# Performance work log

Measured on AMD Instinct MI355X. Metric: run time of the kernel, lower is better.

Reference implementation:

```python
import jax, jax.numpy as jnp
import numpy as np

S, B, CLS = 14, 2, 20
L_COORD, L_NOOBJ = 5.0, 0.5
BATCH = 8192
C = 5 * B + CLS  # 30


def setup_inputs() -> dict:
    key = jax.random.key(0)
    k1, k2, k3 = jax.random.split(key, 3)
    pred = jax.random.normal(k1, (BATCH, S, S, C), dtype=jnp.float32)
    target = jax.random.uniform(k2, (BATCH, S, S, C), dtype=jnp.float32)
    # replicate the conf bit into both box slots (channels 4 and 9)
    obj = (jax.random.uniform(k3, (BATCH, S, S)) > 0.9).astype(jnp.float32)
    target = target.at[..., 4].set(obj)
    target = target.at[..., 9].set(obj)
    return {"pred": pred, "target": target}


def _decode(box5):
    # box5: [..., 5] = (cx, cy, sqrt_w, sqrt_h, conf) -> corners [..., 4]
    x, y, sw, sh = box5[..., 0], box5[..., 1], box5[..., 2], box5[..., 3]
    hw = 0.5 * sw * sw
    hh = 0.5 * sh * sh
    return jnp.stack([x - hw, y - hh, x + hw, y + hh], axis=-1)


def _iou(b1, b2):
    # elementwise IoU over matching rows, like compute_iou with N==M paired rows
    lt = jnp.maximum(b1[..., :2], b2[..., :2])
    rb = jnp.minimum(b1[..., 2:], b2[..., 2:])
    wh = jnp.maximum(rb - lt, 0.0)
    inter = wh[..., 0] * wh[..., 1]
    a1 = (b1[..., 2] - b1[..., 0]) * (b1[..., 3] - b1[..., 1])
    a2 = (b2[..., 2] - b2[..., 0]) * (b2[..., 3] - b2[..., 1])
    denom = a1 + a2 - inter
    safe = jnp.where(denom > 0, denom, 1.0)
    return jnp.where(denom > 0, inter / safe, 0.0)


def reference(pred, target):
    batch = pred.shape[0]
    p = pred.reshape(-1, C)    # [N, 30], N = batch*S*S
    t = target.reshape(-1, C)
    objf = (t[:, 4] > 0).astype(p.dtype)   # [N]
    noobjf = 1.0 - objf

    p_boxes = p[:, :5 * B].reshape(-1, B, 5)   # [N, B, 5]
    t_boxes = t[:, :5 * B].reshape(-1, B, 5)

    iou = _iou(_decode(t_boxes), _decode(p_boxes))   # [N, B]
    max_iou = jnp.max(iou, axis=1)                   # [N]
    max_idx = jnp.argmax(iou, axis=1)                # [N]
    sel = jax.nn.one_hot(max_idx, B, dtype=p.dtype)  # [N, B] response mask
    p_sel = jnp.einsum('nb,nbk->nk', sel, p_boxes)   # [N, 5] responsible pred box
    t_sel = jnp.einsum('nb,nbk->nk', sel, t_boxes)

    # localization: xy + sqrt-wh MSE on responsible box, obj cells only
    local = jnp.sum(objf[:, None] * (p_sel[:, :4] - t_sel[:, :4]) ** 2)
    # classification MSE, obj cells only
    cls_loss = jnp.sum(objf[:, None] * (p[:, 5 * B:] - t[:, 5 * B:]) ** 2)
    # containment: pred conf of responsible box vs (detached) max IoU
    miou_sg = jax.lax.stop_gradient(max_iou)
    contain = jnp.sum(objf * (p_sel[:, 4] - miou_sg) ** 2)
    # no-object: conf of all B boxes in empty cells
    noobj = jnp.sum(noobjf[:, None] * (p_boxes[:, :, 4] - t_boxes[:, :, 4]) ** 2)
    # iou loss: detached max IoU vs target conf of responsible box
    iou_loss = jnp.sum(objf * (miou_sg - t_sel[:, 4]) ** 2)

    loss_all = (L_COORD * local + cls_loss + contain
                + L_NOOBJ * noobj + iou_loss) / batch
    return loss_all
```

## Files before the change

kernel.cpp:

```cpp
#include <hip/hip_runtime.h>

#define SS 14
#define NBOX 2
#define NCLS 20
#define CCH 30

__global__ __launch_bounds__(256) void yolov1_loss_kernel(
    const float* __restrict__ pred, const float* __restrict__ target,
    float* __restrict__ out, int ncells, float inv_batch)
{
    float acc = 0.0f;
    int tid = blockIdx.x * blockDim.x + threadIdx.x;
    int stride = gridDim.x * blockDim.x;

    for (int cell = tid; cell < ncells; cell += stride) {
        const float2* pp = reinterpret_cast<const float2*>(pred + (size_t)cell * CCH);
        const float2* tp = reinterpret_cast<const float2*>(target + (size_t)cell * CCH);
        float p[CCH], t[CCH];
#pragma unroll
        for (int k = 0; k < CCH / 2; ++k) {
            float2 a = pp[k]; p[2 * k] = a.x; p[2 * k + 1] = a.y;
            float2 b = tp[k]; t[2 * k] = b.x; t[2 * k + 1] = b.y;
        }

        float iou0 = 0.f, iou1 = 0.f;
        float loc0 = 0.f, loc1 = 0.f;
#pragma unroll
        for (int b = 0; b < NBOX; ++b) {
            const int o = 5 * b;
            float thw = 0.5f * t[o + 2] * t[o + 2];
            float thh = 0.5f * t[o + 3] * t[o + 3];
            float phw = 0.5f * p[o + 2] * p[o + 2];
            float phh = 0.5f * p[o + 3] * p[o + 3];
            float t0x = t[o + 0] - thw, t0y = t[o + 1] - thh;
            float t1x = t[o + 0] + thw, t1y = t[o + 1] + thh;
            float p0x = p[o + 0] - phw, p0y = p[o + 1] - phh;
            float p1x = p[o + 0] + phw, p1y = p[o + 1] + phh;

            float ltx = fmaxf(t0x, p0x), lty = fmaxf(t0y, p0y);
            float rbx = fminf(t1x, p1x), rby = fminf(t1y, p1y);
            float w = fmaxf(rbx - ltx, 0.0f);
            float h = fmaxf(rby - lty, 0.0f);
            float inter = w * h;
            float a1 = (t1x - t0x) * (t1y - t0y);
            float a2 = (p1x - p0x) * (p1y - p0y);
            float denom = a1 + a2 - inter;
            float iou_b = (denom > 0.0f) ? (inter / denom) : 0.0f;

            float l = 0.0f;
#pragma unroll
            for (int k = 0; k < 4; ++k) {
                float d = p[o + k] - t[o + k];
                l += d * d;
            }
            if (b == 0) { iou0 = iou_b; loc0 = l; }
            else        { iou1 = iou_b; loc1 = l; }
        }

        int sel1 = (iou1 > iou0);
        float max_iou = fmaxf(iou0, iou1);
        float loc   = sel1 ? loc1   : loc0;
        float pconf = sel1 ? p[9]   : p[4];
        float tconf = sel1 ? t[9]   : t[4];

        float cls = 0.0f;
#pragma unroll
        for (int k = 5 * NBOX; k < CCH; ++k) {
            float d = p[k] - t[k];
            cls += d * d;
        }

        float dcon = pconf - max_iou;
        float d4 = p[4] - t[4];
        float d9 = p[9] - t[9];
        float noobj = d4 * d4 + d9 * d9;
        float diou = max_iou - tconf;

        float objf = (t[4] > 0.0f) ? 1.0f : 0.0f;
        acc += objf * (5.0f * loc + cls + dcon * dcon + diou * diou)
             + (1.0f - objf) * 0.5f * noobj;
    }

#pragma unroll
    for (int off = 32; off > 0; off >>= 1)
        acc += __shfl_down(acc, off, 64);

    __shared__ float wsum[4];
    int lane = threadIdx.x & 63;
    int wid = threadIdx.x >> 6;
    if (lane == 0) wsum[wid] = acc;
    __syncthreads();
    if (threadIdx.x == 0) {
        float s = wsum[0] + wsum[1] + wsum[2] + wsum[3];
        atomicAdd(out, s * inv_batch);
    }
}

extern "C" void kernel_launch(void* const* d_in, const int* in_sizes, int n_in,
                              void* d_out, int out_size, void* d_ws, size_t ws_size,
                              hipStream_t stream) {
    const float* pred = (const float*)d_in[0];
    const float* target = (const float*)d_in[1];
    float* out = (float*)d_out;

    int ncells = in_sizes[0] / CCH;
    int batch = ncells / (SS * SS);
    float inv_batch = 1.0f / (float)batch;

    hipMemsetAsync(d_out, 0, sizeof(float) * out_size, stream);

    const int threads = 256;
    int blocks = (ncells + threads - 1) / threads;
    if (blocks > 2048) blocks = 2048;
    yolov1_loss_kernel<<<blocks, threads, 0, stream>>>(pred, target, out,
                                                       ncells, inv_batch);
}
```

Before: 84.17 us.

## Stage per-wave tiles into LDS via global_load_lds with software prefetch

Each wave now copies 64-cell tiles of pred and target straight into LDS with direct global-to-LDS loads, which makes the global reads fully coalesced in place of strided per-thread float2 loads. Once the registers are filled from LDS, the next tile's load is issued so it overlaps the loss math. The grid is fixed at 512 blocks and the block-level shared reduction is replaced by one atomic per wave. In exchange it uses 60KB of LDS per block, which limits occupancy, relies on hand-placed waitcnt instructions, and issues four times as many atomics.

```diff
diff --git a/kernel.cpp b/kernel.cpp
--- a/kernel.cpp
+++ b/kernel.cpp
@@ -2,98 +2,150 @@
 
 #define SS 14
 #define NBOX 2
-#define NCLS 20
 #define CCH 30
+#define TILE_CELLS 64
+#define TILE_FLOATS (TILE_CELLS * CCH)
+#define WAVES_PER_BLOCK 4
+
+typedef __attribute__((address_space(1))) const void as1_void;
+typedef __attribute__((address_space(3))) void as3_void;
+
+__device__ __forceinline__ void stage_tile(const float* __restrict__ g,
+                                           float* l, int lane) {
+    const char* gc = (const char*)g;
+    char* lc = (char*)l;
+#pragma unroll
+    for (int j = 0; j < 7; ++j)
+        __builtin_amdgcn_global_load_lds((as1_void*)(gc + j * 1024 + lane * 16),
+                                         (as3_void*)(lc + j * 1024), 16, 0, 0);
+#pragma unroll
+    for (int j = 0; j < 2; ++j)
+        __builtin_amdgcn_global_load_lds((as1_void*)(gc + 7168 + j * 256 + lane * 4),
+                                         (as3_void*)(lc + 7168 + j * 256), 4, 0, 0);
+}
+
+__device__ __forceinline__ float cell_loss(const float* p, const float* t) {
+    float iou0 = 0.f, iou1 = 0.f, loc0 = 0.f, loc1 = 0.f;
+#pragma unroll
+    for (int b = 0; b < NBOX; ++b) {
+        const int o = 5 * b;
+        float thw = 0.5f * t[o + 2] * t[o + 2];
+        float thh = 0.5f * t[o + 3] * t[o + 3];
+        float phw = 0.5f * p[o + 2] * p[o + 2];
+        float phh = 0.5f * p[o + 3] * p[o + 3];
+        float t0x = t[o + 0] - thw, t0y = t[o + 1] - thh;
+        float t1x = t[o + 0] + thw, t1y = t[o + 1] + thh;
+        float p0x = p[o + 0] - phw, p0y = p[o + 1] - phh;
+        float p1x = p[o + 0] + phw, p1y = p[o + 1] + phh;
+
+        float ltx = fmaxf(t0x, p0x), lty = fmaxf(t0y, p0y);
+        float rbx = fminf(t1x, p1x), rby = fminf(t1y, p1y);
+        float w = fmaxf(rbx - ltx, 0.0f);
+        float h = fmaxf(rby - lty, 0.0f);
+        float inter = w * h;
+        float a1 = (t1x - t0x) * (t1y - t0y);
+        float a2 = (p1x - p0x) * (p1y - p0y);
+        float denom = a1 + a2 - inter;
+        float iou_b = (denom > 0.0f) ? (inter / denom) : 0.0f;
+
+        float l = 0.0f;
+#pragma unroll
+        for (int k = 0; k < 4; ++k) {
+            float d = p[o + k] - t[o + k];
+            l += d * d;
+        }
+        if (b == 0) { iou0 = iou_b; loc0 = l; }
+        else        { iou1 = iou_b; loc1 = l; }
+    }
+
+    int sel1 = (iou1 > iou0);
+    float max_iou = fmaxf(iou0, iou1);
+    float loc   = sel1 ? loc1 : loc0;
+    float pconf = sel1 ? p[9] : p[4];
+    float tconf = sel1 ? t[9] : t[4];
+
+    float cls = 0.0f;
+#pragma unroll
+    for (int k = 5 * NBOX; k < CCH; ++k) {
+        float d = p[k] - t[k];
+        cls += d * d;
+    }
+
+    float dcon = pconf - max_iou;
+    float d4 = p[4] - t[4];
+    float d9 = p[9] - t[9];
+    float noobj = d4 * d4 + d9 * d9;
+    float diou = max_iou - tconf;
+
+    float objf = (t[4] > 0.0f) ? 1.0f : 0.0f;
+    return objf * (5.0f * loc + cls + dcon * dcon + diou * diou)
+         + (1.0f - objf) * 0.5f * noobj;
+}
 
 __global__ __launch_bounds__(256) void yolov1_loss_kernel(
     const float* __restrict__ pred, const float* __restrict__ target,
     float* __restrict__ out, int ncells, float inv_batch)
 {
+    __shared__ __align__(16) float lds[WAVES_PER_BLOCK * 2 * TILE_FLOATS];
+
+    const int lane = threadIdx.x & 63;
+    const int wid  = threadIdx.x >> 6;
+    const int w    = blockIdx.x * WAVES_PER_BLOCK + wid;
+    const int W    = gridDim.x * WAVES_PER_BLOCK;
+    const int ntiles = ncells / TILE_CELLS;
+
+    float* myp = lds + wid * (2 * TILE_FLOATS);
+    float* myt = myp + TILE_FLOATS;
+
     float acc = 0.0f;
-    int tid = blockIdx.x * blockDim.x + threadIdx.x;
-    int stride = gridDim.x * blockDim.x;
+    int tile = w;
+    if (tile < ntiles) {
+        stage_tile(pred   + (size_t)tile * TILE_FLOATS, myp, lane);
+        stage_tile(target + (size_t)tile * TILE_FLOATS, myt, lane);
+        for (;;) {
+            const int next = tile + W;
+            asm volatile("s_waitcnt vmcnt(0)" ::: "memory");
+            __builtin_amdgcn_sched_barrier(0);
 
-    for (int cell = tid; cell < ncells; cell += stride) {
-        const float2* pp = reinterpret_cast<const float2*>(pred + (size_t)cell * CCH);
-        const float2* tp = reinterpret_cast<const float2*>(target + (size_t)cell * CCH);
+            float p[CCH], t[CCH];
+            const float2* pl = (const float2*)(myp + lane * CCH);
+            const float2* tl = (const float2*)(myt + lane * CCH);
+#pragma unroll
+            for (int k = 0; k < CCH / 2; ++k) {
+                float2 a = pl[k]; p[2 * k] = a.x; p[2 * k + 1] = a.y;
+                float2 b = tl[k]; t[2 * k] = b.x; t[2 * k + 1] = b.y;
+            }
+            asm volatile("s_waitcnt lgkmcnt(0)" ::: "memory");
+            __builtin_amdgcn_sched_barrier(0);
+
+            if (next < ntiles) {
+                stage_tile(pred   + (size_t)next * TILE_FLOATS, myp, lane);
+                stage_tile(target + (size_t)next * TILE_FLOATS, myt, lane);
+            }
+            acc += cell_loss(p, t);
+            if (next >= ntiles) break;
+            tile = next;
+        }
+    }
+
+    for (int cell = ntiles * TILE_CELLS + w * 64 + lane; cell < ncells;
+         cell += W * 64) {
         float p[CCH], t[CCH];
+        const float2* pp = (const float2*)(pred + (size_t)cell * CCH);
+        const float2* tp = (const float2*)(target + (size_t)cell * CCH);
 #pragma unroll
         for (int k = 0; k < CCH / 2; ++k) {
             float2 a = pp[k]; p[2 * k] = a.x; p[2 * k + 1] = a.y;
             float2 b = tp[k]; t[2 * k] = b.x; t[2 * k + 1] = b.y;
         }
-
-        float iou0 = 0.f, iou1 = 0.f;
-        float loc0 = 0.f, loc1 = 0.f;
-#pragma unroll
-        for (int b = 0; b < NBOX; ++b) {
-            const int o = 5 * b;
-            float thw = 0.5f * t[o + 2] * t[o + 2];
-            float thh = 0.5f * t[o + 3] * t[o + 3];
-            float phw = 0.5f * p[o + 2] * p[o + 2];
-            float phh = 0.5f * p[o + 3] * p[o + 3];
-            float t0x = t[o + 0] - thw, t0y = t[o + 1] - thh;
-            float t1x = t[o + 0] + thw, t1y = t[o + 1] + thh;
-            float p0x = p[o + 0] - phw, p0y = p[o + 1] - phh;
-            float p1x = p[o + 0] + phw, p1y = p[o + 1] + phh;
-
-            float ltx = fmaxf(t0x, p0x), lty = fmaxf(t0y, p0y);
-            float rbx = fminf(t1x, p1x), rby = fminf(t1y, p1y);
-            float w = fmaxf(rbx - ltx, 0.0f);
-            float h = fmaxf(rby - lty, 0.0f);
-            float inter = w * h;
-            float a1 = (t1x - t0x) * (t1y - t0y);
-            float a2 = (p1x - p0x) * (p1y - p0y);
-            float denom = a1 + a2 - inter;
-            float iou_b = (denom > 0.0f) ? (inter / denom) : 0.0f;
-
-            float l = 0.0f;
-#pragma unroll
-            for (int k = 0; k < 4; ++k) {
-                float d = p[o + k] - t[o + k];
-                l += d * d;
-            }
-            if (b == 0) { iou0 = iou_b; loc0 = l; }
-            else        { iou1 = iou_b; loc1 = l; }
-        }
-
-        int sel1 = (iou1 > iou0);
-        float max_iou = fmaxf(iou0, iou1);
-        float loc   = sel1 ? loc1   : loc0;
-        float pconf = sel1 ? p[9]   : p[4];
-        float tconf = sel1 ? t[9]   : t[4];
-
-        float cls = 0.0f;
-#pragma unroll
-        for (int k = 5 * NBOX; k < CCH; ++k) {
-            float d = p[k] - t[k];
-            cls += d * d;
-        }
-
-        float dcon = pconf - max_iou;
-        float d4 = p[4] - t[4];
-        float d9 = p[9] - t[9];
-        float noobj = d4 * d4 + d9 * d9;
-        float diou = max_iou - tconf;
-
-        float objf = (t[4] > 0.0f) ? 1.0f : 0.0f;
-        acc += objf * (5.0f * loc + cls + dcon * dcon + diou * diou)
-             + (1.0f - objf) * 0.5f * noobj;
+        acc += cell_loss(p, t);
     }
 
 #pragma unroll
     for (int off = 32; off > 0; off >>= 1)
         acc += __shfl_down(acc, off, 64);
-
-    __shared__ float wsum[4];
-    int lane = threadIdx.x & 63;
-    int wid = threadIdx.x >> 6;
-    if (lane == 0) wsum[wid] = acc;
-    __syncthreads();
-    if (threadIdx.x == 0) {
-        float s = wsum[0] + wsum[1] + wsum[2] + wsum[3];
-        atomicAdd(out, s * inv_batch);
-    }
+    if (lane == 0)
+        atomicAdd(out, acc * inv_batch);
 }
 
 extern "C" void kernel_launch(void* const* d_in, const int* in_sizes, int n_in,
@@ -110,8 +162,7 @@
     hipMemsetAsync(d_out, 0, sizeof(float) * out_size, stream);
 
     const int threads = 256;
-    int blocks = (ncells + threads - 1) / threads;
-    if (blocks > 2048) blocks = 2048;
+    int blocks = 512;
     yolov1_loss_kernel<<<blocks, threads, 0, stream>>>(pred, target, out,
                                                        ncells, inv_batch);
 }
```

Measured after the change: 82.77 us. No clear change (-1.7%).
